# Kernel tuning notes

Hardware: AMD Instinct MI355X
Metric: run time of the kernel (lower is better)

The kernel has to match this reference:

```python
import jax, jax.numpy as jnp
import numpy as np

NUM_GRAPHS = 1000
NODES_PER = 100
EDGES_PER = 1600
HIDDEN = 128
NUM_FEATURES = 128
MAX_Z = 1000
NUM_LAYERS = 3
K = 40
LATENT = HIDDEN * NUM_LAYERS + 1  # 385


def setup_inputs() -> dict:
    key = jax.random.key(0)
    ks = jax.random.split(key, 24)
    N = NUM_GRAPHS * NODES_PER
    x = jax.random.normal(ks[0], (N, NUM_FEATURES), dtype=jnp.float32)
    z = jax.random.randint(ks[1], (N,), 0, MAX_Z)
    # intra-graph random edges
    src_l = jax.random.randint(ks[2], (NUM_GRAPHS, EDGES_PER), 0, NODES_PER)
    dst_l = jax.random.randint(ks[3], (NUM_GRAPHS, EDGES_PER), 0, NODES_PER)
    off = (jnp.arange(NUM_GRAPHS) * NODES_PER)[:, None]
    edge_index = jnp.stack([(src_l + off).reshape(-1), (dst_l + off).reshape(-1)], axis=0)
    batch = jnp.repeat(jnp.arange(NUM_GRAPHS), NODES_PER)

    def lin(k, fi, fo):
        return jax.random.normal(k, (fi, fo), dtype=jnp.float32) / np.sqrt(fi)

    fin = NUM_FEATURES + HIDDEN  # 256
    params = dict(
        z_table=jax.random.normal(ks[4], (MAX_Z, HIDDEN), dtype=jnp.float32),
        W0=lin(ks[5], fin, HIDDEN), b0=jnp.zeros((HIDDEN,), jnp.float32),
        W1=lin(ks[6], HIDDEN, HIDDEN), b1=jnp.zeros((HIDDEN,), jnp.float32),
        W2=lin(ks[7], HIDDEN, HIDDEN), b2=jnp.zeros((HIDDEN,), jnp.float32),
        W3=lin(ks[8], HIDDEN, 1), b3=jnp.zeros((1,), jnp.float32),
        cw1=jax.random.normal(ks[9], (16, 1, LATENT), dtype=jnp.float32) / np.sqrt(LATENT),
        cb1=jnp.zeros((16,), jnp.float32),
        cw2=jax.random.normal(ks[10], (32, 16, 5), dtype=jnp.float32) / np.sqrt(16 * 5),
        cb2=jnp.zeros((32,), jnp.float32),
        mW1=lin(ks[11], 512, 128), mb1=jnp.zeros((128,), jnp.float32),
        mW2=lin(ks[12], 128, 1), mb2=jnp.zeros((1,), jnp.float32),
    )
    return dict(x=x, z=z, edge_index=edge_index, batch=batch, **params)


def _conv1d(x, w, b, stride):
    y = jax.lax.conv_general_dilated(x, w, (stride,), 'VALID',
                                     dimension_numbers=('NCH', 'OIH', 'NCH'))
    return y + b[None, :, None]


def _forward(x, z, edge_index, batch, z_table, W0, b0, W1, b1, W2, b2, W3, b3,
             cw1, cb1, cw2, cb2, mW1, mb1, mW2, mb2):
    N = x.shape[0]
    src, dst = edge_index[0], edge_index[1]
    # GCN symmetric normalization (add_self_loops=False)
    deg = jax.ops.segment_sum(jnp.ones(src.shape[0], jnp.float32), dst, num_segments=N)
    dinv = jnp.where(deg > 0, deg ** -0.5, 0.0)
    norm = dinv[src] * dinv[dst]  # [E]

    def gcn(h, W, b):
        hW = h @ W                       # [N, out]
        msg = norm[:, None] * hW[src]    # [E, out]
        return jax.ops.segment_sum(msg, dst, num_segments=N) + b

    h = jnp.concatenate([z_table[z], x], axis=1)  # [N, 256]
    xs = []
    for W, b in ((W0, b0), (W1, b1), (W2, b2), (W3, b3)):
        h = jnp.tanh(gcn(h, W, b))
        xs.append(h)
    feat = jnp.concatenate(xs, axis=-1)  # [N, LATENT]

    # global_sort_pool: sort nodes per graph by last channel, descending, take top-K
    xb = feat.reshape(NUM_GRAPHS, NODES_PER, LATENT)
    order = jnp.argsort(-xb[:, :, -1], axis=1)
    top = jnp.take_along_axis(xb, order[:, :, None], axis=1)[:, :K]  # [B, K, LATENT]

    y = top.reshape(NUM_GRAPHS, 1, K * LATENT)
    y = jax.nn.relu(_conv1d(y, cw1, cb1, LATENT))        # [B, 16, K]
    y = y.reshape(NUM_GRAPHS, 16, K // 2, 2).max(axis=-1)  # maxpool 2,2 -> [B,16,20]
    y = jax.nn.relu(_conv1d(y, cw2, cb2, 1))             # [B, 32, 16]
    y = y.reshape(NUM_GRAPHS, -1)                        # [B, 512]
    y = jax.nn.relu(y @ mW1 + mb1)
    return y @ mW2 + mb2                                 # [B, 1]


def reference(x, z, edge_index, batch, z_table, W0, b0, W1, b1, W2, b2, W3, b3,
              cw1, cb1, cw2, cb2, mW1, mb1, mW2, mb2):
    return _forward(x, z, edge_index, batch, z_table, W0, b0, W1, b1, W2, b2, W3, b3,
                    cw1, cb1, cw2, cb2, mW1, mb1, mW2, mb2)
```

## Files before the change

### kernel.cpp

```cpp
#include <hip/hip_runtime.h>
#include <cstdint>
#include <cstddef>

#define NG     1000
#define NPER   100
#define EPER   1600
#define NNODES (NG*NPER)
#define NEDGES (NG*EPER)
#define HID    128
#define LAT    385
#define FST    388
#define KTOP   40
#define CHG    250
#define NCHUNK 4

__global__ void k_deg(const int* __restrict__ dst, int* __restrict__ deg) {
  int e = blockIdx.x*blockDim.x + threadIdx.x;
  if (e < NEDGES) atomicAdd(&deg[dst[e]], 1);
}

__global__ void k_dinv64(const int* __restrict__ deg, double* __restrict__ dinv) {
  int i = blockIdx.x*blockDim.x + threadIdx.x;
  if (i < NNODES) {
    int d = deg[i];
    dinv[i] = (d > 0) ? 1.0/sqrt((double)d) : 0.0;
  }
}

__global__ __launch_bounds__(128)
void k_csr(const int* __restrict__ ei0, const int* __restrict__ ei1,
           const int* __restrict__ deg,
           int* __restrict__ rowstart, int* __restrict__ csr_s) {
  int g = blockIdx.x;
  int t = threadIdx.x;
  __shared__ int lstart[NPER];
  __shared__ int cursor[NPER];
  __shared__ int ldeg[NPER];
  if (t < NPER) ldeg[t] = deg[g*NPER + t];
  __syncthreads();
  if (t == 0) {
    int run = 0;
    for (int i = 0; i < NPER; ++i) { lstart[i] = run; run += ldeg[i]; }
  }
  __syncthreads();
  if (t < NPER) { rowstart[g*NPER + t] = lstart[t]; cursor[t] = lstart[t]; }
  __syncthreads();
  for (int e = t; e < EPER; e += 128) {
    int ge = g*EPER + e;
    int s = ei0[ge], d = ei1[ge];
    int slot = atomicAdd(&cursor[d - g*NPER], 1);
    csr_s[(size_t)g*EPER + slot] = s - g*NPER;
  }
}

template<bool L0>
__global__ __launch_bounds__(256)
void k_layer64(const double* __restrict__ h_in,
               const int* __restrict__ z, const float* __restrict__ ztab,
               const float* __restrict__ x,
               const float* __restrict__ W, const float* __restrict__ b,
               const int* __restrict__ rowstart, const int* __restrict__ csr_s,
               const double* __restrict__ dinv,
               double* __restrict__ h_out, int gofs) {
  int gl   = blockIdx.x;
  int g    = gofs + gl;
  int half = blockIdx.y;
  int t    = threadIdx.x;
  int cp   = t & 31;
  int ng   = t >> 5;
  int c0   = half*64 + cp*2;

  __shared__ double hW[104][64];
  __shared__ double dinvL[NPER];

  if (t < NPER) dinvL[t] = dinv[g*NPER + t];

  double accx[13], accy[13];
  #pragma unroll
  for (int i = 0; i < 13; ++i) { accx[i] = 0.0; accy[i] = 0.0; }

  int nodeid[13];
  #pragma unroll
  for (int i = 0; i < 13; ++i) {
    int n = ng + 8*i;
    nodeid[i] = (n < NPER) ? n : (NPER-1);
  }

  {
    const double* rp[13];
    const float*  rpf[13];
    #pragma unroll
    for (int i = 0; i < 13; ++i) {
      if (L0) rpf[i] = ztab + (size_t)z[g*NPER + nodeid[i]]*HID;
      else    rp[i]  = h_in + (size_t)(gl*NPER + nodeid[i])*HID;
    }
    for (int k = 0; k < 128; k += 2) {
      float2 wa = *(const float2*)&W[(k  )*HID + c0];
      float2 wb = *(const float2*)&W[(k+1)*HID + c0];
      double wa0 = (double)wa.x, wa1 = (double)wa.y;
      double wb0 = (double)wb.x, wb1 = (double)wb.y;
      #pragma unroll
      for (int i = 0; i < 13; ++i) {
        double h0, h1;
        if (L0) { float2 hf = *(const float2*)&rpf[i][k]; h0 = (double)hf.x; h1 = (double)hf.y; }
        else    { double2 hd = *(const double2*)&rp[i][k]; h0 = hd.x; h1 = hd.y; }
        accx[i] = fma(h0, wa0, accx[i]); accx[i] = fma(h1, wb0, accx[i]);
        accy[i] = fma(h0, wa1, accy[i]); accy[i] = fma(h1, wb1, accy[i]);
      }
    }
  }
  if (L0) {
    const float* rpf[13];
    #pragma unroll
    for (int i = 0; i < 13; ++i)
      rpf[i] = x + (size_t)(g*NPER + nodeid[i])*HID;
    const float* Wx = W + 128*HID;
    for (int k = 0; k < 128; k += 2) {
      float2 wa = *(const float2*)&Wx[(k  )*HID + c0];
      float2 wb = *(const float2*)&Wx[(k+1)*HID + c0];
      double wa0 = (double)wa.x, wa1 = (double)wa.y;
      double wb0 = (double)wb.x, wb1 = (double)wb.y;
      #pragma unroll
      for (int i = 0; i < 13; ++i) {
        float2 hf = *(const float2*)&rpf[i][k];
        double h0 = (double)hf.x, h1 = (double)hf.y;
        accx[i] = fma(h0, wa0, accx[i]); accx[i] = fma(h1, wb0, accx[i]);
        accy[i] = fma(h0, wa1, accy[i]); accy[i] = fma(h1, wb1, accy[i]);
      }
    }
  }
  #pragma unroll
  for (int i = 0; i < 13; ++i) {
    int n = ng + 8*i;
    hW[n][cp*2]   = accx[i];
    hW[n][cp*2+1] = accy[i];
  }
  __syncthreads();

  double bx = (double)b[c0], by = (double)b[c0+1];
  #pragma unroll 1
  for (int i = 0; i < 13; ++i) {
    int n = ng + 8*i;
    if (n < NPER) {
      int gn = g*NPER + n;
      int s0 = rowstart[gn];
      int e1 = (n == NPER-1) ? EPER : rowstart[gn+1];
      double dd = dinvL[n];
      double sx = 0.0, sy = 0.0;
      for (int e = s0; e < e1; ++e) {
        int    s  = csr_s[(size_t)g*EPER + e];
        double nm = dinvL[s]*dd;
        sx = fma(nm, hW[s][cp*2],   sx);
        sy = fma(nm, hW[s][cp*2+1], sy);
      }
      size_t o = (size_t)(gl*NPER + n)*HID + c0;
      h_out[o]   = tanh(sx + bx);
      h_out[o+1] = tanh(sy + by);
    }
  }
}

__global__ __launch_bounds__(128)
void k_l3sel(const double* __restrict__ h2, const float* __restrict__ W3,
             const float* __restrict__ b3,
             const int* __restrict__ rowstart, const int* __restrict__ csr_s,
             const double* __restrict__ dinv,
             double* __restrict__ key64, int* __restrict__ sel, int gofs) {
  int gl = blockIdx.x, g = gofs + gl, t = threadIdx.x;
  __shared__ double w3d[128];
  __shared__ double hv[NPER];
  __shared__ double key[NPER];
  __shared__ double dinvL[NPER];
  if (t < 128) w3d[t] = (double)W3[t];
  if (t < NPER) dinvL[t] = dinv[g*NPER + t];
  __syncthreads();
  if (t < NPER) {
    const double* row = h2 + (size_t)(gl*NPER + t)*HID;
    double s = 0.0;
    for (int k = 0; k < 128; ++k) s = fma(row[k], w3d[k], s);
    hv[t] = s;
  }
  __syncthreads();
  if (t < NPER) {
    int gn = g*NPER + t;
    int s0 = rowstart[gn];
    int e1 = (t == NPER-1) ? EPER : rowstart[gn+1];
    double dd = dinvL[t];
    double sum = 0.0;
    for (int e = s0; e < e1; ++e) {
      int s = csr_s[(size_t)g*EPER + e];
      sum = fma(dinvL[s]*dd, hv[s], sum);
    }
    double kv = tanh(sum + (double)b3[0]);
    key[t] = kv;
    key64[gl*NPER + t] = kv;
  }
  __syncthreads();
  if (t < NPER) {
    double ki = key[t];
    int rank = 0;
    for (int j = 0; j < NPER; ++j) {
      double kj = key[j];
      rank += ((kj > ki) || (kj == ki && j < t)) ? 1 : 0;
    }
    if (rank < KTOP) sel[g*KTOP + rank] = g*NPER + t;
  }
}

__global__ __launch_bounds__(256)
void k_gather(const double* __restrict__ h0, const double* __restrict__ h1,
              const double* __restrict__ h2, const double* __restrict__ key64,
              const int* __restrict__ sel, float* __restrict__ topf, int gofs) {
  int gl = blockIdx.x, g = gofs + gl, t = threadIdx.x;
  for (int idx = t; idx < KTOP*97; idx += 256) {
    int k = idx / 97, q = idx - k*97;
    int nloc = sel[g*KTOP + k] - g*NPER;
    size_t row = (size_t)(gl*NPER + nloc)*HID;
    float4 v;
    if (q < 96) {
      const double* src = (q < 32) ? &h0[row + q*4]
                        : (q < 64) ? &h1[row + (q-32)*4]
                                   : &h2[row + (q-64)*4];
      double2 a = *(const double2*)src;
      double2 c = *(const double2*)(src + 2);
      v = make_float4((float)a.x, (float)a.y, (float)c.x, (float)c.y);
    } else {
      v = make_float4((float)key64[gl*NPER + nloc], 0.f, 0.f, 0.f);
    }
    *(float4*)&topf[((size_t)g*KTOP + k)*FST + q*4] = v;
  }
}

__global__ __launch_bounds__(256)
void k_head(const float* __restrict__ topf,
            const float* __restrict__ cw1, const float* __restrict__ cb1,
            const float* __restrict__ cw2, const float* __restrict__ cb2,
            const float* __restrict__ mW1, const float* __restrict__ mb1,
            const float* __restrict__ mW2, const float* __restrict__ mb2,
            float* __restrict__ out) {
  int g = blockIdx.x, t = threadIdx.x;
  __shared__ float4 top4[KTOP*97];
  __shared__ float  c1t[LAT*16];
  __shared__ float  y1s[16*KTOP];
  __shared__ float  pools[16*20];
  __shared__ float  y2s[512];
  __shared__ float  m1s[128];
  float* top = (float*)top4;

  const float4* tp = (const float4*)topf;
  for (int idx = t; idx < KTOP*97; idx += 256)
    top4[idx] = tp[(size_t)g*KTOP*97 + idx];
  for (int idx = t; idx < LAT*16; idx += 256) {
    int l = idx >> 4, f = idx & 15;
    c1t[idx] = cw1[f*LAT + l];
  }
  __syncthreads();
  for (int idx = t; idx < 16*KTOP; idx += 256) {
    int f = idx & 15, k = idx >> 4;
    float acc = cb1[f];
    for (int l = 0; l < LAT; ++l)
      acc = fmaf(top[k*FST + l], c1t[l*16 + f], acc);
    y1s[f*KTOP + k] = fmaxf(acc, 0.f);
  }
  __syncthreads();
  for (int idx = t; idx < 16*20; idx += 256) {
    int f = idx / 20, tt = idx % 20;
    pools[idx] = fmaxf(y1s[f*KTOP + 2*tt], y1s[f*KTOP + 2*tt + 1]);
  }
  __syncthreads();
  for (int idx = t; idx < 512; idx += 256) {
    int c = idx >> 4, tt = idx & 15;
    float acc = cb2[c];
    #pragma unroll
    for (int f = 0; f < 16; ++f)
      #pragma unroll
      for (int j = 0; j < 5; ++j)
        acc = fmaf(cw2[c*80 + f*5 + j], pools[f*20 + tt + j], acc);
    y2s[idx] = fmaxf(acc, 0.f);
  }
  __syncthreads();
  if (t < 128) {
    float acc = mb1[t];
    for (int i = 0; i < 512; ++i)
      acc = fmaf(y2s[i], mW1[i*128 + t], acc);
    m1s[t] = fmaxf(acc, 0.f);
  }
  __syncthreads();
  if (t < 64) {
    float v = fmaf(m1s[t], mW2[t], m1s[t+64]*mW2[t+64]);
    #pragma unroll
    for (int off = 32; off > 0; off >>= 1) v += __shfl_down(v, off);
    if (t == 0) out[g] = v + mb2[0];
  }
}

extern "C" void kernel_launch(void* const* d_in, const int* in_sizes, int n_in,
                              void* d_out, int out_size, void* d_ws, size_t ws_size,
                              hipStream_t stream) {
  const float* x    = (const float*)d_in[0];
  const int*   z    = (const int*)  d_in[1];
  const int*   ei   = (const int*)  d_in[2];
  const float* ztab = (const float*)d_in[4];
  const float* W0   = (const float*)d_in[5];
  const float* b0   = (const float*)d_in[6];
  const float* W1   = (const float*)d_in[7];
  const float* b1   = (const float*)d_in[8];
  const float* W2   = (const float*)d_in[9];
  const float* b2   = (const float*)d_in[10];
  const float* W3   = (const float*)d_in[11];
  const float* b3   = (const float*)d_in[12];
  const float* cw1  = (const float*)d_in[13];
  const float* cb1  = (const float*)d_in[14];
  const float* cw2  = (const float*)d_in[15];
  const float* cb2  = (const float*)d_in[16];
  const float* mW1  = (const float*)d_in[17];
  const float* mb1  = (const float*)d_in[18];
  const float* mW2  = (const float*)d_in[19];
  const float* mb2  = (const float*)d_in[20];
  float* out = (float*)d_out;

  char* ws = (char*)d_ws;
  size_t off = 0;
  auto alloc = [&](size_t bytes) {
    void* p = ws + off;
    off = (off + bytes + 255) & ~(size_t)255;
    return p;
  };
  int*    deg      = (int*)   alloc((size_t)NNODES*4);
  double* dinv     = (double*)alloc((size_t)NNODES*8);
  int*    rowstart = (int*)   alloc((size_t)NNODES*4);
  int*    csr_s    = (int*)   alloc((size_t)NEDGES*4);
  int*    sel      = (int*)   alloc((size_t)NG*KTOP*4);
  double* key64    = (double*)alloc((size_t)CHG*NPER*8);
  double* h0       = (double*)alloc((size_t)CHG*NPER*HID*8);
  double* h1       = (double*)alloc((size_t)CHG*NPER*HID*8);
  double* h2       = (double*)alloc((size_t)CHG*NPER*HID*8);
  float*  topf     = (float*) alloc((size_t)NG*KTOP*FST*4);
  (void)ws_size;

  const int* ei0 = ei;
  const int* ei1 = ei + NEDGES;

  hipMemsetAsync(deg, 0, (size_t)NNODES*4, stream);
  k_deg   <<<(NEDGES+255)/256, 256, 0, stream>>>(ei1, deg);
  k_dinv64<<<(NNODES+255)/256, 256, 0, stream>>>(deg, dinv);
  k_csr   <<<NG, 128, 0, stream>>>(ei0, ei1, deg, rowstart, csr_s);

  for (int c = 0; c < NCHUNK; ++c) {
    int gofs = c*CHG;
    dim3 lg(CHG, 2);
    k_layer64<true ><<<lg, 256, 0, stream>>>(h0, z, ztab, x, W0, b0, rowstart, csr_s, dinv, h0, gofs);
    k_layer64<false><<<lg, 256, 0, stream>>>(h0, z, ztab, x, W1, b1, rowstart, csr_s, dinv, h1, gofs);
    k_layer64<false><<<lg, 256, 0, stream>>>(h1, z, ztab, x, W2, b2, rowstart, csr_s, dinv, h2, gofs);
    k_l3sel<<<CHG, 128, 0, stream>>>(h2, W3, b3, rowstart, csr_s, dinv, key64, sel, gofs);
    k_gather<<<CHG, 256, 0, stream>>>(h0, h1, h2, key64, sel, topf, gofs);
  }
  k_head<<<NG, 256, 0, stream>>>(topf, cw1, cb1, cw2, cb2, mW1, mb1, mW2, mb2, out);
}
```

Before: 1.900 ms.

## Split fused GCN layer into separate node-parallel GEMM and aggregation kernels

Replaces the fused per-graph layer kernel, where each thread held 13 node accumulators, with two kernels. A flat GEMM kernel computes h·W for 16 nodes per block into a global buffer, and an aggregation kernel loads a 32-column slice of that result into shared memory and does the CSR neighbor sum plus tanh. Chunk size also changes from 250 to 200 graphs. The aim is to cut register pressure and raise occupancy and parallelism for the FP64 GEMM. The cost is an extra global round trip of the hW intermediate and more kernel launches.

```diff
diff --git a/kernel.cpp b/kernel.cpp
--- a/kernel.cpp
+++ b/kernel.cpp
@@ -11,8 +11,10 @@
 #define LAT    385
 #define FST    388
 #define KTOP   40
-#define CHG    250
-#define NCHUNK 4
+#define CHG    200
+#define NCHUNK 5
+#define CHN    (CHG*NPER)
+#define GEMM_BLOCKS (CHN/16)
 
 __global__ void k_deg(const int* __restrict__ dst, int* __restrict__ deg) {
   int e = blockIdx.x*blockDim.x + threadIdx.x;
@@ -55,86 +57,103 @@
 
 template<bool L0>
 __global__ __launch_bounds__(256)
-void k_layer64(const double* __restrict__ h_in,
-               const int* __restrict__ z, const float* __restrict__ ztab,
-               const float* __restrict__ x,
-               const float* __restrict__ W, const float* __restrict__ b,
-               const int* __restrict__ rowstart, const int* __restrict__ csr_s,
-               const double* __restrict__ dinv,
-               double* __restrict__ h_out, int gofs) {
-  int gl   = blockIdx.x;
-  int g    = gofs + gl;
-  int half = blockIdx.y;
-  int t    = threadIdx.x;
-  int cp   = t & 31;
-  int ng   = t >> 5;
-  int c0   = half*64 + cp*2;
-
-  __shared__ double hW[104][64];
+void k_gemm64(const double* __restrict__ h_in,
+              const int* __restrict__ z, const float* __restrict__ ztab,
+              const float* __restrict__ x,
+              const float* __restrict__ W,
+              double* __restrict__ hW, int nofs) {
+  int t  = threadIdx.x;
+  int cq = t & 31;
+  int ng = t >> 5;
+  int c0 = cq*4;
+  int n0 = blockIdx.x*16 + ng;
+  int n1 = n0 + 8;
+
+  double a00=0,a01=0,a02=0,a03=0;
+  double a10=0,a11=0,a12=0,a13=0;
+
+  {
+    const float  *zr0, *zr1;
+    const double *r0, *r1;
+    if (L0) {
+      zr0 = ztab + (size_t)z[nofs + n0]*HID;
+      zr1 = ztab + (size_t)z[nofs + n1]*HID;
+    } else {
+      r0 = h_in + (size_t)n0*HID;
+      r1 = h_in + (size_t)n1*HID;
+    }
+    #pragma unroll 2
+    for (int k = 0; k < 128; k += 2) {
+      float4 wa = *(const float4*)&W[(k  )*HID + c0];
+      float4 wb = *(const float4*)&W[(k+1)*HID + c0];
+      double h0, h1;
+      if (L0) { float2 hf = *(const float2*)&zr0[k]; h0 = (double)hf.x; h1 = (double)hf.y; }
+      else    { double2 hd = *(const double2*)&r0[k]; h0 = hd.x; h1 = hd.y; }
+      a00 = fma(h0,(double)wa.x,a00); a00 = fma(h1,(double)wb.x,a00);
+      a01 = fma(h0,(double)wa.y,a01); a01 = fma(h1,(double)wb.y,a01);
+      a02 = fma(h0,(double)wa.z,a02); a02 = fma(h1,(double)wb.z,a02);
+      a03 = fma(h0,(double)wa.w,a03); a03 = fma(h1,(double)wb.w,a03);
+      if (L0) { float2 hf = *(const float2*)&zr1[k]; h0 = (double)hf.x; h1 = (double)hf.y; }
+      else    { double2 hd = *(const double2*)&r1[k]; h0 = hd.x; h1 = hd.y; }
+      a10 = fma(h0,(double)wa.x,a10); a10 = fma(h1,(double)wb.x,a10);
+      a11 = fma(h0,(double)wa.y,a11); a11 = fma(h1,(double)wb.y,a11);
+      a12 = fma(h0,(double)wa.z,a12); a12 = fma(h1,(double)wb.z,a12);
+      a13 = fma(h0,(double)wa.w,a13); a13 = fma(h1,(double)wb.w,a13);
+    }
+  }
+  if (L0) {
+    const float* xr0 = x + (size_t)(nofs + n0)*HID;
+    const float* xr1 = x + (size_t)(nofs + n1)*HID;
+    const float* Wx = W + 128*HID;
+    #pragma unroll 2
+    for (int k = 0; k < 128; k += 2) {
+      float4 wa = *(const float4*)&Wx[(k  )*HID + c0];
+      float4 wb = *(const float4*)&Wx[(k+1)*HID + c0];
+      float2 hf = *(const float2*)&xr0[k];
+      double h0 = (double)hf.x, h1 = (double)hf.y;
+      a00 = fma(h0,(double)wa.x,a00); a00 = fma(h1,(double)wb.x,a00);
+      a01 = fma(h0,(double)wa.y,a01); a01 = fma(h1,(double)wb.y,a01);
+      a02 = fma(h0,(double)wa.z,a02); a02 = fma(h1,(double)wb.z,a02);
+      a03 = fma(h0,(double)wa.w,a03); a03 = fma(h1,(double)wb.w,a03);
+      hf = *(const float2*)&xr1[k];
+      h0 = (double)hf.x; h1 = (double)hf.y;
+      a10 = fma(h0,(double)wa.x,a10); a10 = fma(h1,(double)wb.x,a10);
+      a11 = fma(h0,(double)wa.y,a11); a11 = fma(h1,(double)wb.y,a11);
+      a12 = fma(h0,(double)wa.z,a12); a12 = fma(h1,(double)wb.z,a12);
+      a13 = fma(h0,(double)wa.w,a13); a13 = fma(h1,(double)wb.w,a13);
+    }
+  }
+  double2 s;
+  s.x=a00; s.y=a01; *(double2*)&hW[(size_t)n0*HID + c0]     = s;
+  s.x=a02; s.y=a03; *(double2*)&hW[(size_t)n0*HID + c0 + 2] = s;
+  s.x=a10; s.y=a11; *(double2*)&hW[(size_t)n1*HID + c0]     = s;
+  s.x=a12; s.y=a13; *(double2*)&hW[(size_t)n1*HID + c0 + 2] = s;
+}
+
+__global__ __launch_bounds__(128)
+void k_agg64(const double* __restrict__ hW, const float* __restrict__ b,
+             const int* __restrict__ rowstart, const int* __restrict__ csr_s,
+             const double* __restrict__ dinv,
+             double* __restrict__ h_out, int gofs) {
+  int gl = blockIdx.x;
+  int q  = blockIdx.y;
+  int g  = gofs + gl;
+  int t  = threadIdx.x;
+  int cp = t & 15;
+  int ng = t >> 4;
+  int cq0 = q*32;
+  int c0  = cq0 + cp*2;
+
+  __shared__ double hWs[NPER][34];
   __shared__ double dinvL[NPER];
 
+  for (int idx = t; idx < NPER*16; idx += 128) {
+    int row = idx >> 4, p = idx & 15;
+    double2 v = *(const double2*)&hW[(size_t)(gl*NPER + row)*HID + cq0 + p*2];
+    hWs[row][p*2]   = v.x;
+    hWs[row][p*2+1] = v.y;
+  }
   if (t < NPER) dinvL[t] = dinv[g*NPER + t];
-
-  double accx[13], accy[13];
-  #pragma unroll
-  for (int i = 0; i < 13; ++i) { accx[i] = 0.0; accy[i] = 0.0; }
-
-  int nodeid[13];
-  #pragma unroll
-  for (int i = 0; i < 13; ++i) {
-    int n = ng + 8*i;
-    nodeid[i] = (n < NPER) ? n : (NPER-1);
-  }
-
-  {
-    const double* rp[13];
-    const float*  rpf[13];
-    #pragma unroll
-    for (int i = 0; i < 13; ++i) {
-      if (L0) rpf[i] = ztab + (size_t)z[g*NPER + nodeid[i]]*HID;
-      else    rp[i]  = h_in + (size_t)(gl*NPER + nodeid[i])*HID;
-    }
-    for (int k = 0; k < 128; k += 2) {
-      float2 wa = *(const float2*)&W[(k  )*HID + c0];
-      float2 wb = *(const float2*)&W[(k+1)*HID + c0];
-      double wa0 = (double)wa.x, wa1 = (double)wa.y;
-      double wb0 = (double)wb.x, wb1 = (double)wb.y;
-      #pragma unroll
-      for (int i = 0; i < 13; ++i) {
-        double h0, h1;
-        if (L0) { float2 hf = *(const float2*)&rpf[i][k]; h0 = (double)hf.x; h1 = (double)hf.y; }
-        else    { double2 hd = *(const double2*)&rp[i][k]; h0 = hd.x; h1 = hd.y; }
-        accx[i] = fma(h0, wa0, accx[i]); accx[i] = fma(h1, wb0, accx[i]);
-        accy[i] = fma(h0, wa1, accy[i]); accy[i] = fma(h1, wb1, accy[i]);
-      }
-    }
-  }
-  if (L0) {
-    const float* rpf[13];
-    #pragma unroll
-    for (int i = 0; i < 13; ++i)
-      rpf[i] = x + (size_t)(g*NPER + nodeid[i])*HID;
-    const float* Wx = W + 128*HID;
-    for (int k = 0; k < 128; k += 2) {
-      float2 wa = *(const float2*)&Wx[(k  )*HID + c0];
-      float2 wb = *(const float2*)&Wx[(k+1)*HID + c0];
-      double wa0 = (double)wa.x, wa1 = (double)wa.y;
-      double wb0 = (double)wb.x, wb1 = (double)wb.y;
-      #pragma unroll
-      for (int i = 0; i < 13; ++i) {
-        float2 hf = *(const float2*)&rpf[i][k];
-        double h0 = (double)hf.x, h1 = (double)hf.y;
-        accx[i] = fma(h0, wa0, accx[i]); accx[i] = fma(h1, wb0, accx[i]);
-        accy[i] = fma(h0, wa1, accy[i]); accy[i] = fma(h1, wb1, accy[i]);
-      }
-    }
-  }
-  #pragma unroll
-  for (int i = 0; i < 13; ++i) {
-    int n = ng + 8*i;
-    hW[n][cp*2]   = accx[i];
-    hW[n][cp*2+1] = accy[i];
-  }
   __syncthreads();
 
   double bx = (double)b[c0], by = (double)b[c0+1];
@@ -150,12 +169,12 @@
       for (int e = s0; e < e1; ++e) {
         int    s  = csr_s[(size_t)g*EPER + e];
         double nm = dinvL[s]*dd;
-        sx = fma(nm, hW[s][cp*2],   sx);
-        sy = fma(nm, hW[s][cp*2+1], sy);
+        sx = fma(nm, hWs[s][cp*2],   sx);
+        sy = fma(nm, hWs[s][cp*2+1], sy);
       }
       size_t o = (size_t)(gl*NPER + n)*HID + c0;
-      h_out[o]   = tanh(sx + bx);
-      h_out[o+1] = tanh(sy + by);
+      double2 v; v.x = tanh(sx + bx); v.y = tanh(sy + by);
+      *(double2*)&h_out[o] = v;
     }
   }
 }
@@ -331,10 +350,11 @@
   int*    rowstart = (int*)   alloc((size_t)NNODES*4);
   int*    csr_s    = (int*)   alloc((size_t)NEDGES*4);
   int*    sel      = (int*)   alloc((size_t)NG*KTOP*4);
-  double* key64    = (double*)alloc((size_t)CHG*NPER*8);
-  double* h0       = (double*)alloc((size_t)CHG*NPER*HID*8);
-  double* h1       = (double*)alloc((size_t)CHG*NPER*HID*8);
-  double* h2       = (double*)alloc((size_t)CHG*NPER*HID*8);
+  double* key64    = (double*)alloc((size_t)CHN*8);
+  double* h0       = (double*)alloc((size_t)CHN*HID*8);
+  double* h1       = (double*)alloc((size_t)CHN*HID*8);
+  double* h2       = (double*)alloc((size_t)CHN*HID*8);
+  double* hWb      = (double*)alloc((size_t)CHN*HID*8);
   float*  topf     = (float*) alloc((size_t)NG*KTOP*FST*4);
   (void)ws_size;
 
@@ -348,11 +368,15 @@
 
   for (int c = 0; c < NCHUNK; ++c) {
     int gofs = c*CHG;
-    dim3 lg(CHG, 2);
-    k_layer64<true ><<<lg, 256, 0, stream>>>(h0, z, ztab, x, W0, b0, rowstart, csr_s, dinv, h0, gofs);
-    k_layer64<false><<<lg, 256, 0, stream>>>(h0, z, ztab, x, W1, b1, rowstart, csr_s, dinv, h1, gofs);
-    k_layer64<false><<<lg, 256, 0, stream>>>(h1, z, ztab, x, W2, b2, rowstart, csr_s, dinv, h2, gofs);
-    k_l3sel<<<CHG, 128, 0, stream>>>(h2, W3, b3, rowstart, csr_s, dinv, key64, sel, gofs);
+    int nofs = gofs*NPER;
+    dim3 gB(CHG, 4);
+    k_gemm64<true ><<<GEMM_BLOCKS, 256, 0, stream>>>(h0, z, ztab, x, W0, hWb, nofs);
+    k_agg64 <<<gB, 128, 0, stream>>>(hWb, b0, rowstart, csr_s, dinv, h0, gofs);
+    k_gemm64<false><<<GEMM_BLOCKS, 256, 0, stream>>>(h0, z, ztab, x, W1, hWb, nofs);
+    k_agg64 <<<gB, 128, 0, stream>>>(hWb, b1, rowstart, csr_s, dinv, h1, gofs);
+    k_gemm64<false><<<GEMM_BLOCKS, 256, 0, stream>>>(h1, z, ztab, x, W2, hWb, nofs);
+    k_agg64 <<<gB, 128, 0, stream>>>(hWb, b2, rowstart, csr_s, dinv, h2, gofs);
+    k_l3sel <<<CHG, 128, 0, stream>>>(h2, W3, b3, rowstart, csr_s, dinv, key64, sel, gofs);
     k_gather<<<CHG, 256, 0, stream>>>(h0, h1, h2, key64, sel, topf, gofs);
   }
   k_head<<<NG, 256, 0, stream>>>(topf, cw1, cb1, cw2, cb2, mW1, mb1, mW2, mb2, out);
```

Result: slower. 1.989 ms (+4.7%).

## Split GCN layers into quarter-column blocks, stage CSR in LDS, fuse select+gather

Applied to the files above, without the earlier changes.

The GCN layer kernel now splits the 128 output columns into four 32-column blocks per graph instead of two. Each block uses 16 node groups with 7 nodes per thread, and sets launch bounds for 4 blocks per CU to raise occupancy and parallelism. The per-graph CSR edge list and row starts are staged in shared memory, and outputs are written as double2. Layer-3 key computation, top-K selection and the gather into topf are fused into one kernel, which removes the sel and key64 buffers. The head kernel now reads topf rows directly from global memory with float4 loads instead of staging them in LDS. The cost is that each block redundantly loads the inputs for its column slice, and head reads become uncached global loads.

```diff
diff --git a/kernel.cpp b/kernel.cpp
--- a/kernel.cpp
+++ b/kernel.cpp
@@ -13,6 +13,7 @@
 #define KTOP   40
 #define CHG    250
 #define NCHUNK 4
+#define CHN    (CHG*NPER)
 
 __global__ void k_deg(const int* __restrict__ dst, int* __restrict__ deg) {
   int e = blockIdx.x*blockDim.x + threadIdx.x;
@@ -54,7 +55,7 @@
 }
 
 template<bool L0>
-__global__ __launch_bounds__(256)
+__global__ __launch_bounds__(256, 4)
 void k_layer64(const double* __restrict__ h_in,
                const int* __restrict__ z, const float* __restrict__ ztab,
                const float* __restrict__ x,
@@ -62,117 +63,120 @@
                const int* __restrict__ rowstart, const int* __restrict__ csr_s,
                const double* __restrict__ dinv,
                double* __restrict__ h_out, int gofs) {
-  int gl   = blockIdx.x;
-  int g    = gofs + gl;
-  int half = blockIdx.y;
-  int t    = threadIdx.x;
-  int cp   = t & 31;
-  int ng   = t >> 5;
-  int c0   = half*64 + cp*2;
-
-  __shared__ double hW[104][64];
+  int gl = blockIdx.x;
+  int q  = blockIdx.y;
+  int g  = gofs + gl;
+  int t  = threadIdx.x;
+  int cp = t & 15;
+  int ng = t >> 4;
+  int c0 = q*32 + cp*2;
+
+  __shared__ double hWs[NPER][34];
   __shared__ double dinvL[NPER];
-
-  if (t < NPER) dinvL[t] = dinv[g*NPER + t];
-
-  double accx[13], accy[13];
+  __shared__ int    rsL[NPER+1];
+  __shared__ int    edgeL[EPER];
+
+  for (int e = t; e < EPER; e += 256) edgeL[e] = csr_s[(size_t)g*EPER + e];
+  if (t < NPER) { dinvL[t] = dinv[g*NPER + t]; rsL[t] = rowstart[g*NPER + t]; }
+  else if (t == NPER) rsL[NPER] = EPER;
+
+  int nid[7];
   #pragma unroll
-  for (int i = 0; i < 13; ++i) { accx[i] = 0.0; accy[i] = 0.0; }
-
-  int nodeid[13];
+  for (int i = 0; i < 7; ++i) { int n = ng + 16*i; nid[i] = (n < NPER) ? n : (NPER-1); }
+
+  double ax[7], ay[7];
   #pragma unroll
-  for (int i = 0; i < 13; ++i) {
-    int n = ng + 8*i;
-    nodeid[i] = (n < NPER) ? n : (NPER-1);
-  }
+  for (int i = 0; i < 7; ++i) { ax[i] = 0.0; ay[i] = 0.0; }
 
   {
-    const double* rp[13];
-    const float*  rpf[13];
+    const double* rp[7];
+    const float*  rpf[7];
     #pragma unroll
-    for (int i = 0; i < 13; ++i) {
-      if (L0) rpf[i] = ztab + (size_t)z[g*NPER + nodeid[i]]*HID;
-      else    rp[i]  = h_in + (size_t)(gl*NPER + nodeid[i])*HID;
+    for (int i = 0; i < 7; ++i) {
+      if (L0) rpf[i] = ztab + (size_t)z[g*NPER + nid[i]]*HID;
+      else    rp[i]  = h_in + (size_t)(gl*NPER + nid[i])*HID;
     }
     for (int k = 0; k < 128; k += 2) {
       float2 wa = *(const float2*)&W[(k  )*HID + c0];
       float2 wb = *(const float2*)&W[(k+1)*HID + c0];
-      double wa0 = (double)wa.x, wa1 = (double)wa.y;
-      double wb0 = (double)wb.x, wb1 = (double)wb.y;
+      double wax = (double)wa.x, way = (double)wa.y;
+      double wbx = (double)wb.x, wby = (double)wb.y;
       #pragma unroll
-      for (int i = 0; i < 13; ++i) {
-        double h0, h1;
-        if (L0) { float2 hf = *(const float2*)&rpf[i][k]; h0 = (double)hf.x; h1 = (double)hf.y; }
-        else    { double2 hd = *(const double2*)&rp[i][k]; h0 = hd.x; h1 = hd.y; }
-        accx[i] = fma(h0, wa0, accx[i]); accx[i] = fma(h1, wb0, accx[i]);
-        accy[i] = fma(h0, wa1, accy[i]); accy[i] = fma(h1, wb1, accy[i]);
+      for (int i = 0; i < 7; ++i) {
+        double h0v, h1v;
+        if (L0) { float2 hf = *(const float2*)&rpf[i][k]; h0v = (double)hf.x; h1v = (double)hf.y; }
+        else    { double2 hd = *(const double2*)&rp[i][k]; h0v = hd.x; h1v = hd.y; }
+        ax[i] = fma(h0v, wax, ax[i]); ax[i] = fma(h1v, wbx, ax[i]);
+        ay[i] = fma(h0v, way, ay[i]); ay[i] = fma(h1v, wby, ay[i]);
       }
     }
   }
   if (L0) {
-    const float* rpf[13];
+    const float* rpf[7];
     #pragma unroll
-    for (int i = 0; i < 13; ++i)
-      rpf[i] = x + (size_t)(g*NPER + nodeid[i])*HID;
+    for (int i = 0; i < 7; ++i) rpf[i] = x + (size_t)(g*NPER + nid[i])*HID;
     const float* Wx = W + 128*HID;
     for (int k = 0; k < 128; k += 2) {
       float2 wa = *(const float2*)&Wx[(k  )*HID + c0];
       float2 wb = *(const float2*)&Wx[(k+1)*HID + c0];
-      double wa0 = (double)wa.x, wa1 = (double)wa.y;
-      double wb0 = (double)wb.x, wb1 = (double)wb.y;
+      double wax = (double)wa.x, way = (double)wa.y;
+      double wbx = (double)wb.x, wby = (double)wb.y;
       #pragma unroll
-      for (int i = 0; i < 13; ++i) {
+      for (int i = 0; i < 7; ++i) {
         float2 hf = *(const float2*)&rpf[i][k];
-        double h0 = (double)hf.x, h1 = (double)hf.y;
-        accx[i] = fma(h0, wa0, accx[i]); accx[i] = fma(h1, wb0, accx[i]);
-        accy[i] = fma(h0, wa1, accy[i]); accy[i] = fma(h1, wb1, accy[i]);
+        double h0v = (double)hf.x, h1v = (double)hf.y;
+        ax[i] = fma(h0v, wax, ax[i]); ax[i] = fma(h1v, wbx, ax[i]);
+        ay[i] = fma(h0v, way, ay[i]); ay[i] = fma(h1v, wby, ay[i]);
       }
     }
   }
   #pragma unroll
-  for (int i = 0; i < 13; ++i) {
-    int n = ng + 8*i;
-    hW[n][cp*2]   = accx[i];
-    hW[n][cp*2+1] = accy[i];
+  for (int i = 0; i < 7; ++i) {
+    int n = ng + 16*i;
+    if (n < NPER) { hWs[n][cp*2] = ax[i]; hWs[n][cp*2+1] = ay[i]; }
   }
   __syncthreads();
 
   double bx = (double)b[c0], by = (double)b[c0+1];
   #pragma unroll 1
-  for (int i = 0; i < 13; ++i) {
-    int n = ng + 8*i;
+  for (int i = 0; i < 7; ++i) {
+    int n = ng + 16*i;
     if (n < NPER) {
-      int gn = g*NPER + n;
-      int s0 = rowstart[gn];
-      int e1 = (n == NPER-1) ? EPER : rowstart[gn+1];
+      int s0 = rsL[n], e1 = rsL[n+1];
       double dd = dinvL[n];
       double sx = 0.0, sy = 0.0;
       for (int e = s0; e < e1; ++e) {
-        int    s  = csr_s[(size_t)g*EPER + e];
+        int    s  = edgeL[e];
         double nm = dinvL[s]*dd;
-        sx = fma(nm, hW[s][cp*2],   sx);
-        sy = fma(nm, hW[s][cp*2+1], sy);
+        sx = fma(nm, hWs[s][cp*2],   sx);
+        sy = fma(nm, hWs[s][cp*2+1], sy);
       }
       size_t o = (size_t)(gl*NPER + n)*HID + c0;
-      h_out[o]   = tanh(sx + bx);
-      h_out[o+1] = tanh(sy + by);
+      double2 v; v.x = tanh(sx + bx); v.y = tanh(sy + by);
+      *(double2*)&h_out[o] = v;
     }
   }
 }
 
 __global__ __launch_bounds__(128)
-void k_l3sel(const double* __restrict__ h2, const float* __restrict__ W3,
-             const float* __restrict__ b3,
-             const int* __restrict__ rowstart, const int* __restrict__ csr_s,
-             const double* __restrict__ dinv,
-             double* __restrict__ key64, int* __restrict__ sel, int gofs) {
+void k_l3g(const double* __restrict__ h0, const double* __restrict__ h1,
+           const double* __restrict__ h2,
+           const float* __restrict__ W3, const float* __restrict__ b3,
+           const int* __restrict__ rowstart, const int* __restrict__ csr_s,
+           const double* __restrict__ dinv,
+           float* __restrict__ topf, int gofs) {
   int gl = blockIdx.x, g = gofs + gl, t = threadIdx.x;
   __shared__ double w3d[128];
   __shared__ double hv[NPER];
   __shared__ double key[NPER];
   __shared__ double dinvL[NPER];
-  if (t < 128) w3d[t] = (double)W3[t];
-  if (t < NPER) dinvL[t] = dinv[g*NPER + t];
+  __shared__ int    rsL[NPER+1];
+  __shared__ int    edgeL[EPER];
+  __shared__ int    selL[KTOP];
+  for (int e = t; e < EPER; e += 128) edgeL[e] = csr_s[(size_t)g*EPER + e];
+  w3d[t] = (double)W3[t];
+  if (t < NPER) { dinvL[t] = dinv[g*NPER + t]; rsL[t] = rowstart[g*NPER + t]; }
+  else if (t == NPER) rsL[NPER] = EPER;
   __syncthreads();
   if (t < NPER) {
     const double* row = h2 + (size_t)(gl*NPER + t)*HID;
@@ -182,18 +186,14 @@
   }
   __syncthreads();
   if (t < NPER) {
-    int gn = g*NPER + t;
-    int s0 = rowstart[gn];
-    int e1 = (t == NPER-1) ? EPER : rowstart[gn+1];
     double dd = dinvL[t];
     double sum = 0.0;
+    int s0 = rsL[t], e1 = rsL[t+1];
     for (int e = s0; e < e1; ++e) {
-      int s = csr_s[(size_t)g*EPER + e];
+      int s = edgeL[e];
       sum = fma(dinvL[s]*dd, hv[s], sum);
     }
-    double kv = tanh(sum + (double)b3[0]);
-    key[t] = kv;
-    key64[gl*NPER + t] = kv;
+    key[t] = tanh(sum + (double)b3[0]);
   }
   __syncthreads();
   if (t < NPER) {
@@ -203,31 +203,25 @@
       double kj = key[j];
       rank += ((kj > ki) || (kj == ki && j < t)) ? 1 : 0;
     }
-    if (rank < KTOP) sel[g*KTOP + rank] = g*NPER + t;
-  }
-}
-
-__global__ __launch_bounds__(256)
-void k_gather(const double* __restrict__ h0, const double* __restrict__ h1,
-              const double* __restrict__ h2, const double* __restrict__ key64,
-              const int* __restrict__ sel, float* __restrict__ topf, int gofs) {
-  int gl = blockIdx.x, g = gofs + gl, t = threadIdx.x;
-  for (int idx = t; idx < KTOP*97; idx += 256) {
-    int k = idx / 97, q = idx - k*97;
-    int nloc = sel[g*KTOP + k] - g*NPER;
+    if (rank < KTOP) selL[rank] = t;
+  }
+  __syncthreads();
+  for (int idx = t; idx < KTOP*97; idx += 128) {
+    int k = idx / 97, qq = idx - k*97;
+    int nloc = selL[k];
     size_t row = (size_t)(gl*NPER + nloc)*HID;
     float4 v;
-    if (q < 96) {
-      const double* src = (q < 32) ? &h0[row + q*4]
-                        : (q < 64) ? &h1[row + (q-32)*4]
-                                   : &h2[row + (q-64)*4];
+    if (qq < 96) {
+      const double* src = (qq < 32) ? &h0[row + qq*4]
+                        : (qq < 64) ? &h1[row + (qq-32)*4]
+                                    : &h2[row + (qq-64)*4];
       double2 a = *(const double2*)src;
       double2 c = *(const double2*)(src + 2);
       v = make_float4((float)a.x, (float)a.y, (float)c.x, (float)c.y);
     } else {
-      v = make_float4((float)key64[gl*NPER + nloc], 0.f, 0.f, 0.f);
-    }
-    *(float4*)&topf[((size_t)g*KTOP + k)*FST + q*4] = v;
+      v = make_float4((float)key[nloc], 0.f, 0.f, 0.f);
+    }
+    *(float4*)&topf[((size_t)g*KTOP + k)*FST + qq*4] = v;
   }
 }
 
@@ -239,27 +233,31 @@
             const float* __restrict__ mW2, const float* __restrict__ mb2,
             float* __restrict__ out) {
   int g = blockIdx.x, t = threadIdx.x;
-  __shared__ float4 top4[KTOP*97];
-  __shared__ float  c1t[LAT*16];
-  __shared__ float  y1s[16*KTOP];
-  __shared__ float  pools[16*20];
-  __shared__ float  y2s[512];
-  __shared__ float  m1s[128];
-  float* top = (float*)top4;
-
-  const float4* tp = (const float4*)topf;
-  for (int idx = t; idx < KTOP*97; idx += 256)
-    top4[idx] = tp[(size_t)g*KTOP*97 + idx];
+  __shared__ float c1t[LAT*16];
+  __shared__ float y1s[16*KTOP];
+  __shared__ float pools[16*20];
+  __shared__ float y2s[512];
+  __shared__ float m1s[128];
+
   for (int idx = t; idx < LAT*16; idx += 256) {
     int l = idx >> 4, f = idx & 15;
     c1t[idx] = cw1[f*LAT + l];
   }
   __syncthreads();
+  const float* tg = topf + (size_t)g*KTOP*FST;
   for (int idx = t; idx < 16*KTOP; idx += 256) {
     int f = idx & 15, k = idx >> 4;
+    const float4* row4 = (const float4*)(tg + (size_t)k*FST);
     float acc = cb1[f];
-    for (int l = 0; l < LAT; ++l)
-      acc = fmaf(top[k*FST + l], c1t[l*16 + f], acc);
+    for (int l4 = 0; l4 < 96; ++l4) {
+      float4 r = row4[l4];
+      const float* cc = &c1t[(l4*4)*16 + f];
+      acc = fmaf(r.x, cc[0],  acc);
+      acc = fmaf(r.y, cc[16], acc);
+      acc = fmaf(r.z, cc[32], acc);
+      acc = fmaf(r.w, cc[48], acc);
+    }
+    acc = fmaf(tg[(size_t)k*FST + 384], c1t[384*16 + f], acc);
     y1s[f*KTOP + k] = fmaxf(acc, 0.f);
   }
   __syncthreads();
@@ -330,11 +328,9 @@
   double* dinv     = (double*)alloc((size_t)NNODES*8);
   int*    rowstart = (int*)   alloc((size_t)NNODES*4);
   int*    csr_s    = (int*)   alloc((size_t)NEDGES*4);
-  int*    sel      = (int*)   alloc((size_t)NG*KTOP*4);
-  double* key64    = (double*)alloc((size_t)CHG*NPER*8);
-  double* h0       = (double*)alloc((size_t)CHG*NPER*HID*8);
-  double* h1       = (double*)alloc((size_t)CHG*NPER*HID*8);
-  double* h2       = (double*)alloc((size_t)CHG*NPER*HID*8);
+  double* h0       = (double*)alloc((size_t)CHN*HID*8);
+  double* h1       = (double*)alloc((size_t)CHN*HID*8);
+  double* h2       = (double*)alloc((size_t)CHN*HID*8);
   float*  topf     = (float*) alloc((size_t)NG*KTOP*FST*4);
   (void)ws_size;
 
@@ -348,12 +344,11 @@
 
   for (int c = 0; c < NCHUNK; ++c) {
     int gofs = c*CHG;
-    dim3 lg(CHG, 2);
+    dim3 lg(CHG, 4);
     k_layer64<true ><<<lg, 256, 0, stream>>>(h0, z, ztab, x, W0, b0, rowstart, csr_s, dinv, h0, gofs);
     k_layer64<false><<<lg, 256, 0, stream>>>(h0, z, ztab, x, W1, b1, rowstart, csr_s, dinv, h1, gofs);
     k_layer64<false><<<lg, 256, 0, stream>>>(h1, z, ztab, x, W2, b2, rowstart, csr_s, dinv, h2, gofs);
-    k_l3sel<<<CHG, 128, 0, stream>>>(h2, W3, b3, rowstart, csr_s, dinv, key64, sel, gofs);
-    k_gather<<<CHG, 256, 0, stream>>>(h0, h1, h2, key64, sel, topf, gofs);
+    k_l3g   <<<CHG, 128, 0, stream>>>(h0, h1, h2, W3, b3, rowstart, csr_s, dinv, topf, gofs);
   }
   k_head<<<NG, 256, 0, stream>>>(topf, cw1, cb1, cw2, cb2, mW1, mb1, mW2, mb2, out);
 }
```

Result: faster. 1.728 ms (-9.1%).
